# Performance work log

Measured on AMD Instinct MI355X. Metric: run time of the kernel, lower is better.

The kernel has to match this reference:

```python
import jax, jax.numpy as jnp
import numpy as np

N = 50000      # nodes
E = 800000     # edges (avg degree 16)
F_IN = 512
HID = 128
OUT = 40
DROPOUT = 0.5


def setup_inputs() -> dict:
    key = jax.random.key(0)
    ks = jax.random.split(key, 9)
    x = jax.random.normal(ks[0], (N, F_IN), dtype=jnp.float32)
    edge_src = jax.random.randint(ks[1], (E,), 0, N, dtype=jnp.int32)
    edge_dst = jax.random.randint(ks[2], (E,), 0, N, dtype=jnp.int32)
    edge_weight = jax.random.uniform(ks[3], (E,), dtype=jnp.float32)
    # GraphConvolution params (Glorot-ish init like the torch reference)
    s1 = 1.0 / np.sqrt(HID)
    W1 = jax.random.uniform(ks[4], (F_IN, HID), minval=-s1, maxval=s1, dtype=jnp.float32)
    b1 = jax.random.uniform(ks[5], (HID,), minval=-s1, maxval=s1, dtype=jnp.float32)
    s2 = 1.0 / np.sqrt(OUT)
    W2 = jax.random.uniform(ks[6], (HID, OUT), minval=-s2, maxval=s2, dtype=jnp.float32)
    b2 = jax.random.uniform(ks[7], (OUT,), minval=-s2, maxval=s2, dtype=jnp.float32)
    # Pre-sampled dropout mask (training-mode dropout, deterministic reference):
    keep = jax.random.bernoulli(ks[8], 1.0 - DROPOUT, (N, HID))
    drop_mask = keep.astype(jnp.float32) / (1.0 - DROPOUT)
    return {"x": x, "W1": W1, "b1": b1, "W2": W2, "b2": b2,
            "edge_weight": edge_weight, "drop_mask": drop_mask,
            "edge_src": edge_src, "edge_dst": edge_dst}


def spmm(edge_src, edge_dst, edge_weight, h):
    # out[i] = sum_{e: dst_e = i} w_e * h[src_e]   (sparse adj @ h)
    msgs = edge_weight[:, None] * h[edge_src]      # [E, d]
    return jax.ops.segment_sum(msgs, edge_dst, num_segments=N)


def reference(x, W1, b1, W2, b2, edge_weight, drop_mask, edge_src, edge_dst):
    # layer 1: adj @ (x @ W1) + b1, relu, dropout
    h = spmm(edge_src, edge_dst, edge_weight, x @ W1) + b1
    h = jax.nn.relu(h) * drop_mask
    # layer 2: adj @ (h @ W2) + b2
    out = spmm(edge_src, edge_dst, edge_weight, h @ W2) + b2
    return out
```

## Files before the change

### kernel.cpp

```cpp
#include <hip/hip_runtime.h>

#define NN 50000
#define NE 800000
#define FIN 512
#define HID 128
#define NOUT 40
#define H2P 64
#define CAP 64
#define NXS 16
#define GB1 782
#define EPB 2048
#define SB  391
#define MB  782

typedef __bf16 v8bf __attribute__((ext_vector_type(8)));
typedef float  v4f  __attribute__((ext_vector_type(4)));
typedef float  v2f  __attribute__((ext_vector_type(2)));
typedef unsigned short us8 __attribute__((ext_vector_type(8)));
typedef unsigned short us4 __attribute__((ext_vector_type(4)));
typedef unsigned int   u32x4 __attribute__((ext_vector_type(4)));
typedef unsigned int   u32x2 __attribute__((ext_vector_type(2)));

static __device__ __forceinline__ unsigned short f2bf(float f) {
  union { float f; unsigned int u; } v; v.f = f;
  unsigned int r = v.u + 0x7FFFu + ((v.u >> 16) & 1u);
  return (unsigned short)(r >> 16);
}
static __device__ __forceinline__ float bf2f(unsigned short s) {
  union { unsigned int u; float f; } v; v.u = ((unsigned int)s) << 16;
  return v.f;
}
static __device__ __forceinline__ float u2f(unsigned int u) {
  union { unsigned int u; float f; } v; v.u = u;
  return v.f;
}
static __device__ __forceinline__ v2f bfp2f(unsigned int u) {
  v2f r; r.x = u2f(u << 16); r.y = u2f(u & 0xFFFF0000u); return r;
}

__global__ void k_w1t(const float* __restrict__ W1, unsigned short* __restrict__ W1t,
                      int* __restrict__ nxt) {
  int id = blockIdx.x * 256 + threadIdx.x;
  int k = id >> 7;
  int n = id & 127;
  W1t[n * FIN + k] = f2bf(W1[k * HID + n]);
  if (id < NN) nxt[(size_t)id * NXS] = 0;
}

#define BM1 64
#define BK1 64
#define BKP1 72
__global__ __launch_bounds__(256) void k_fused(
    const float* __restrict__ x, const unsigned short* __restrict__ W1t,
    unsigned short* __restrict__ hb0,
    const int* __restrict__ src, const int* __restrict__ dst,
    const float* __restrict__ w, int* __restrict__ nxt,
    unsigned int* __restrict__ bkt,
    const float* __restrict__ mask, unsigned int* __restrict__ mpk) {
  __shared__ unsigned short As[BM1 * BKP1];
  __shared__ unsigned short Bs[HID * BKP1];
  const int t = threadIdx.x;

  if (blockIdx.x >= GB1 + SB) {
    int id = (blockIdx.x - (GB1 + SB)) * 256 + t;
    if (id < NN * 4) {
      int row = id >> 2, seg = id & 3;
      const float4* mp = (const float4*)(mask + (size_t)row * HID + seg * 32);
      unsigned int bits = 0;
      #pragma unroll
      for (int q = 0; q < 8; ++q) {
        float4 v = mp[q];
        bits |= (v.x != 0.f ? 1u : 0u) << (q * 4);
        bits |= (v.y != 0.f ? 1u : 0u) << (q * 4 + 1);
        bits |= (v.z != 0.f ? 1u : 0u) << (q * 4 + 2);
        bits |= (v.w != 0.f ? 1u : 0u) << (q * 4 + 3);
      }
      mpk[(size_t)row * 4 + seg] = bits;
    }
    return;
  }

  if (blockIdx.x >= GB1) {
    const int base = (blockIdx.x - GB1) * EPB + t;
    int   ii[8]; unsigned int pk[8]; int ok[8];
    #pragma unroll
    for (int k = 0; k < 8; ++k) {
      int e = base + k * 256;
      ok[k] = (e < NE);
      int ec = ok[k] ? e : (NE - 1);
      ii[k] = dst[ec];
      pk[k] = (unsigned int)src[ec] | ((unsigned int)f2bf(w[ec]) << 16);
    }
    int p[8];
    #pragma unroll
    for (int k = 0; k < 8; ++k)
      p[k] = ok[k] ? atomicAdd(&nxt[(size_t)ii[k] * NXS], 1) : CAP;
    #pragma unroll
    for (int k = 0; k < 8; ++k)
      if (p[k] < CAP) bkt[(size_t)ii[k] * CAP + p[k]] = pk[k];
    return;
  }

  const int r0 = blockIdx.x * BM1;
  const int wave = t >> 6, lane = t & 63;
  const int quad = lane >> 4, mr = lane & 15;
  const int mrow0 = (wave & 1) * 32;
  const int ncol0 = (wave >> 1) * 64;

  const int ar = t >> 2, aq = t & 3;
  int grow = r0 + ar; if (grow > NN - 1) grow = NN - 1;
  const float4* xrow = (const float4*)(x + (size_t)grow * FIN);
  const int bn = t >> 1, bh = t & 1;

  const v4f vzero = {0.f, 0.f, 0.f, 0.f};
  v4f acc[2][4];
  #pragma unroll
  for (int mi = 0; mi < 2; ++mi)
    #pragma unroll
    for (int j = 0; j < 4; ++j) acc[mi][j] = vzero;

  for (int k0 = 0; k0 < FIN; k0 += BK1) {
    float4 va[4];
    #pragma unroll
    for (int i = 0; i < 4; ++i) va[i] = xrow[(k0 >> 2) + aq + i * 4];
    us8 vb[4];
    const us8* bp = (const us8*)(W1t + bn * FIN + k0 + bh * 32);
    #pragma unroll
    for (int i = 0; i < 4; ++i) vb[i] = bp[i];

    __syncthreads();
    #pragma unroll
    for (int i = 0; i < 4; ++i) {
      us4 s; s.x = f2bf(va[i].x); s.y = f2bf(va[i].y);
             s.z = f2bf(va[i].z); s.w = f2bf(va[i].w);
      *(us4*)&As[ar * BKP1 + aq * 4 + i * 16] = s;
    }
    #pragma unroll
    for (int i = 0; i < 4; ++i)
      *(us8*)&Bs[bn * BKP1 + bh * 32 + i * 8] = vb[i];
    __syncthreads();

    #pragma unroll
    for (int ks = 0; ks < BK1; ks += 32) {
      v8bf a0 = *(const v8bf*)&As[(mrow0 + mr) * BKP1 + ks + quad * 8];
      v8bf a1 = *(const v8bf*)&As[(mrow0 + 16 + mr) * BKP1 + ks + quad * 8];
      #pragma unroll
      for (int j = 0; j < 4; ++j) {
        v8bf b = *(const v8bf*)&Bs[(ncol0 + j * 16 + mr) * BKP1 + ks + quad * 8];
        acc[0][j] = __builtin_amdgcn_mfma_f32_16x16x32_bf16(a0, b, acc[0][j], 0, 0, 0);
        acc[1][j] = __builtin_amdgcn_mfma_f32_16x16x32_bf16(a1, b, acc[1][j], 0, 0, 0);
      }
    }
  }

  #pragma unroll
  for (int mi = 0; mi < 2; ++mi)
    #pragma unroll
    for (int j = 0; j < 4; ++j)
      #pragma unroll
      for (int rr = 0; rr < 4; ++rr) {
        int row = r0 + mrow0 + mi * 16 + quad * 4 + rr;
        int col = ncol0 + j * 16 + mr;
        if (row < NN) hb0[(size_t)row * HID + col] = f2bf(acc[mi][j][rr]);
      }
}

__global__ __launch_bounds__(256) void k_spmm1(const unsigned short* __restrict__ hb0,
                                               const int* __restrict__ nxt,
                                               const unsigned int* __restrict__ bkt,
                                               const float* __restrict__ b1,
                                               const unsigned int* __restrict__ mpk,
                                               unsigned short* __restrict__ hb1) {
  const int t = threadIdx.x, lane = t & 63, wv = t >> 6;
  const int g = lane >> 4, ql = lane & 15;
  const int i = blockIdx.x * 4 + wv;
  const int c0 = ql * 8;
  int nE = nxt[(size_t)i * NXS]; if (nE > CAP) nE = CAP;
  const int m = (nE + 3 - g) >> 2;
  const unsigned int* ep = bkt + (size_t)i * CAP + g;

  const v2f z2 = {0.f, 0.f};
  v2f a0p[4] = {z2, z2, z2, z2};
  v2f a1p[4] = {z2, z2, z2, z2};
  int j = 0;
  for (; j + 3 < m; j += 4) {
    unsigned int p0 = ep[4*j], p1 = ep[4*j+4], p2 = ep[4*j+8], p3 = ep[4*j+12];
    int s0 = p0 & 0xFFFF, s1 = p1 & 0xFFFF, s2 = p2 & 0xFFFF, s3 = p3 & 0xFFFF;
    v2f w0 = {0.f, 0.f}, w1 = w0, w2 = w0, w3 = w0;
    w0.x = w0.y = bf2f((unsigned short)(p0 >> 16));
    w1.x = w1.y = bf2f((unsigned short)(p1 >> 16));
    w2.x = w2.y = bf2f((unsigned short)(p2 >> 16));
    w3.x = w3.y = bf2f((unsigned short)(p3 >> 16));
    u32x4 h0 = *(const u32x4*)&hb0[(size_t)s0 * HID + c0];
    u32x4 h1 = *(const u32x4*)&hb0[(size_t)s1 * HID + c0];
    u32x4 h2 = *(const u32x4*)&hb0[(size_t)s2 * HID + c0];
    u32x4 h3 = *(const u32x4*)&hb0[(size_t)s3 * HID + c0];
    #pragma unroll
    for (int d = 0; d < 4; ++d) {
      a0p[d] += w0 * bfp2f(h0[d]);
      a1p[d] += w1 * bfp2f(h1[d]);
      a0p[d] += w2 * bfp2f(h2[d]);
      a1p[d] += w3 * bfp2f(h3[d]);
    }
  }
  for (; j < m; ++j) {
    unsigned int p = ep[4*j];
    int s = p & 0xFFFF;
    v2f w; w.x = w.y = bf2f((unsigned short)(p >> 16));
    u32x4 h = *(const u32x4*)&hb0[(size_t)s * HID + c0];
    #pragma unroll
    for (int d = 0; d < 4; ++d) a0p[d] += w * bfp2f(h[d]);
  }
  float v[8];
  #pragma unroll
  for (int d = 0; d < 4; ++d) {
    v2f s = a0p[d] + a1p[d];
    v[2*d] = s.x; v[2*d+1] = s.y;
  }
  #pragma unroll
  for (int k = 0; k < 8; ++k) {
    v[k] += __shfl_xor(v[k], 16);
    v[k] += __shfl_xor(v[k], 32);
  }
  if (g == 0) {
    unsigned int word = mpk[(size_t)i * 4 + (ql >> 2)];
    unsigned int byte = (word >> ((ql & 3) * 8)) & 0xFFu;
    const float4 bbA = *(const float4*)&b1[c0];
    const float4 bbB = *(const float4*)&b1[c0 + 4];
    float bb[8] = {bbA.x, bbA.y, bbA.z, bbA.w, bbB.x, bbB.y, bbB.z, bbB.w};
    us8 o;
    #pragma unroll
    for (int k = 0; k < 8; ++k) {
      float r = ((byte >> k) & 1u) ? fmaxf(v[k] + bb[k], 0.f) * 2.0f : 0.f;
      o[k] = f2bf(r);
    }
    *(us8*)&hb1[(size_t)i * HID + c0] = o;
  }
}

#define BKP2 136
__global__ __launch_bounds__(256) void k_gemm2(const unsigned short* __restrict__ hb1,
                                               const float* __restrict__ W2,
                                               unsigned short* __restrict__ h2b) {
  __shared__ unsigned short As[64 * BKP2];
  __shared__ unsigned short Bs[48 * BKP2];
  const int t = threadIdx.x;
  const int r0 = blockIdx.x * 64;
  const int wave = t >> 6, lane = t & 63;
  const int quad = lane >> 4, mr = lane & 15;
  const int mrow0 = wave * 16;

  const int ar = t >> 2, aq = t & 3;
  int grow = r0 + ar; if (grow > NN - 1) grow = NN - 1;
  const us8* hrow = (const us8*)(hb1 + (size_t)grow * HID);
  #pragma unroll
  for (int i = 0; i < 4; ++i) {
    us8 v = hrow[aq + i * 4];
    *(us8*)&As[ar * BKP2 + aq * 8 + i * 32] = v;
  }
  if (t < 192) {
    int n = t >> 2, q = t & 3;
    #pragma unroll
    for (int kk = 0; kk < 32; ++kk) {
      int k = q * 32 + kk;
      float val = (n < NOUT) ? W2[k * NOUT + n] : 0.f;
      Bs[n * BKP2 + k] = f2bf(val);
    }
  }
  __syncthreads();

  const v4f vzero = {0.f, 0.f, 0.f, 0.f};
  v4f acc[3] = {vzero, vzero, vzero};
  #pragma unroll
  for (int ks = 0; ks < HID; ks += 32) {
    v8bf a = *(const v8bf*)&As[(mrow0 + mr) * BKP2 + ks + quad * 8];
    #pragma unroll
    for (int j = 0; j < 3; ++j) {
      v8bf b = *(const v8bf*)&Bs[(j * 16 + mr) * BKP2 + ks + quad * 8];
      acc[j] = __builtin_amdgcn_mfma_f32_16x16x32_bf16(a, b, acc[j], 0, 0, 0);
    }
  }
  #pragma unroll
  for (int j = 0; j < 3; ++j)
    #pragma unroll
    for (int rr = 0; rr < 4; ++rr) {
      int row = r0 + mrow0 + quad * 4 + rr;
      int col = j * 16 + mr;
      if (row < NN && col < NOUT) h2b[(size_t)row * H2P + col] = f2bf(acc[j][rr]);
    }
}

__global__ __launch_bounds__(256) void k_spmm2(const unsigned short* __restrict__ h2b,
                                               const int* __restrict__ nxt,
                                               const unsigned int* __restrict__ bkt,
                                               const float* __restrict__ b2,
                                               float* __restrict__ out) {
  const int t = threadIdx.x, lane = t & 63;
  const int g = lane >> 4, ql = lane & 15;
  const int i = blockIdx.x * 4 + (t >> 6);
  if (i >= NN) return;
  const int act = (ql < 10);
  const int c0 = act ? ql * 4 : 0;
  int nE = nxt[(size_t)i * NXS]; if (nE > CAP) nE = CAP;
  const int m = (nE + 3 - g) >> 2;
  const unsigned int* ep = bkt + (size_t)i * CAP + g;

  const v2f z2 = {0.f, 0.f};
  v2f a0p[2] = {z2, z2};
  v2f a1p[2] = {z2, z2};
  int j = 0;
  for (; j + 3 < m; j += 4) {
    unsigned int p0 = ep[4*j], p1 = ep[4*j+4], p2 = ep[4*j+8], p3 = ep[4*j+12];
    int s0 = p0 & 0xFFFF, s1 = p1 & 0xFFFF, s2 = p2 & 0xFFFF, s3 = p3 & 0xFFFF;
    v2f w0, w1, w2, w3;
    w0.x = w0.y = bf2f((unsigned short)(p0 >> 16));
    w1.x = w1.y = bf2f((unsigned short)(p1 >> 16));
    w2.x = w2.y = bf2f((unsigned short)(p2 >> 16));
    w3.x = w3.y = bf2f((unsigned short)(p3 >> 16));
    u32x2 h0 = *(const u32x2*)&h2b[(size_t)s0 * H2P + c0];
    u32x2 h1 = *(const u32x2*)&h2b[(size_t)s1 * H2P + c0];
    u32x2 h2 = *(const u32x2*)&h2b[(size_t)s2 * H2P + c0];
    u32x2 h3 = *(const u32x2*)&h2b[(size_t)s3 * H2P + c0];
    #pragma unroll
    for (int d = 0; d < 2; ++d) {
      a0p[d] += w0 * bfp2f(h0[d]);
      a1p[d] += w1 * bfp2f(h1[d]);
      a0p[d] += w2 * bfp2f(h2[d]);
      a1p[d] += w3 * bfp2f(h3[d]);
    }
  }
  for (; j < m; ++j) {
    unsigned int p = ep[4*j];
    int s = p & 0xFFFF;
    v2f w; w.x = w.y = bf2f((unsigned short)(p >> 16));
    u32x2 h = *(const u32x2*)&h2b[(size_t)s * H2P + c0];
    #pragma unroll
    for (int d = 0; d < 2; ++d) a0p[d] += w * bfp2f(h[d]);
  }
  float v[4];
  #pragma unroll
  for (int d = 0; d < 2; ++d) {
    v2f s = a0p[d] + a1p[d];
    v[2*d] = s.x; v[2*d+1] = s.y;
  }
  #pragma unroll
  for (int k = 0; k < 4; ++k) {
    v[k] += __shfl_xor(v[k], 16);
    v[k] += __shfl_xor(v[k], 32);
  }
  if (g == 0 && act) {
    const float4 bb = *(const float4*)&b2[c0];
    float4 o;
    o.x = v[0] + bb.x;
    o.y = v[1] + bb.y;
    o.z = v[2] + bb.z;
    o.w = v[3] + bb.w;
    *(float4*)&out[(size_t)i * NOUT + c0] = o;
  }
}

extern "C" void kernel_launch(void* const* d_in, const int* in_sizes, int n_in,
                              void* d_out, int out_size, void* d_ws, size_t ws_size,
                              hipStream_t stream) {
  const float* x   = (const float*)d_in[0];
  const float* W1  = (const float*)d_in[1];
  const float* b1  = (const float*)d_in[2];
  const float* W2  = (const float*)d_in[3];
  const float* b2  = (const float*)d_in[4];
  const float* ew  = (const float*)d_in[5];
  const float* msk = (const float*)d_in[6];
  const int* esrc  = (const int*)d_in[7];
  const int* edst  = (const int*)d_in[8];
  float* out = (float*)d_out;

  char* ws = (char*)d_ws;
  unsigned short* hb0 = (unsigned short*)ws; ws += (size_t)NN * HID * 2;
  unsigned short* hb1 = (unsigned short*)ws; ws += (size_t)NN * HID * 2;
  unsigned short* h2b = (unsigned short*)ws; ws += (size_t)NN * H2P * 2;
  unsigned short* W1t = (unsigned short*)ws; ws += (size_t)HID * FIN * 2;
  unsigned int* bkt   = (unsigned int*)ws;   ws += (size_t)NN * CAP * 4;
  unsigned int* mpk   = (unsigned int*)ws;   ws += (size_t)NN * 4 * 4;
  int* nxt            = (int*)ws;            ws += (size_t)NN * NXS * 4;

  k_w1t  <<<(FIN * HID) / 256, 256, 0, stream>>>(W1, W1t, nxt);
  k_fused<<<GB1 + SB + MB, 256, 0, stream>>>(x, W1t, hb0,
                                             esrc, edst, ew, nxt, bkt,
                                             msk, mpk);
  k_spmm1<<<NN / 4, 256, 0, stream>>>(hb0, nxt, bkt, b1, mpk, hb1);
  k_gemm2<<<(NN + 63) / 64, 256, 0, stream>>>(hb1, W2, h2b);
  k_spmm2<<<(NN + 3) / 4, 256, 0, stream>>>(h2b, nxt, bkt, b2, out);
}
```

Measured before the change: 295.4 us.

## Load GEMM operands directly from global into MFMA registers, dropping LDS staging

The x@W1 GEMM in the fused kernel no longer stages tiles of x and W1t through shared memory with barriers. Each lane now loads its own MFMA fragments straight from global memory, converting x to bf16 in registers, over a fully unrolled K loop. This removes LDS traffic and __syncthreads, but the two waves sharing a row slice (or column slice) each fetch it from global, relying on cache for reuse. The per-lane accesses are also less coalesced (16-byte chunks spread across rows) and register pressure rises from the full unroll.

```diff
diff --git a/kernel.cpp b/kernel.cpp
--- a/kernel.cpp
+++ b/kernel.cpp
@@ -48,8 +48,6 @@
 }
 
 #define BM1 64
-#define BK1 64
-#define BKP1 72
 __global__ __launch_bounds__(256) void k_fused(
     const float* __restrict__ x, const unsigned short* __restrict__ W1t,
     unsigned short* __restrict__ hb0,
@@ -57,8 +55,6 @@
     const float* __restrict__ w, int* __restrict__ nxt,
     unsigned int* __restrict__ bkt,
     const float* __restrict__ mask, unsigned int* __restrict__ mpk) {
-  __shared__ unsigned short As[BM1 * BKP1];
-  __shared__ unsigned short Bs[HID * BKP1];
   const int t = threadIdx.x;
 
   if (blockIdx.x >= GB1 + SB) {
@@ -107,10 +103,14 @@
   const int mrow0 = (wave & 1) * 32;
   const int ncol0 = (wave >> 1) * 64;
 
-  const int ar = t >> 2, aq = t & 3;
-  int grow = r0 + ar; if (grow > NN - 1) grow = NN - 1;
-  const float4* xrow = (const float4*)(x + (size_t)grow * FIN);
-  const int bn = t >> 1, bh = t & 1;
+  int rA0 = r0 + mrow0 + mr;      if (rA0 > NN - 1) rA0 = NN - 1;
+  int rA1 = r0 + mrow0 + 16 + mr; if (rA1 > NN - 1) rA1 = NN - 1;
+  const float* xr0 = x + (size_t)rA0 * FIN;
+  const float* xr1 = x + (size_t)rA1 * FIN;
+  const unsigned short* wb0 = W1t + (size_t)(ncol0 + 0 * 16 + mr) * FIN;
+  const unsigned short* wb1 = W1t + (size_t)(ncol0 + 1 * 16 + mr) * FIN;
+  const unsigned short* wb2 = W1t + (size_t)(ncol0 + 2 * 16 + mr) * FIN;
+  const unsigned short* wb3 = W1t + (size_t)(ncol0 + 3 * 16 + mr) * FIN;
 
   const v4f vzero = {0.f, 0.f, 0.f, 0.f};
   v4f acc[2][4];
@@ -119,38 +119,34 @@
     #pragma unroll
     for (int j = 0; j < 4; ++j) acc[mi][j] = vzero;
 
-  for (int k0 = 0; k0 < FIN; k0 += BK1) {
-    float4 va[4];
-    #pragma unroll
-    for (int i = 0; i < 4; ++i) va[i] = xrow[(k0 >> 2) + aq + i * 4];
-    us8 vb[4];
-    const us8* bp = (const us8*)(W1t + bn * FIN + k0 + bh * 32);
-    #pragma unroll
-    for (int i = 0; i < 4; ++i) vb[i] = bp[i];
-
-    __syncthreads();
-    #pragma unroll
-    for (int i = 0; i < 4; ++i) {
-      us4 s; s.x = f2bf(va[i].x); s.y = f2bf(va[i].y);
-             s.z = f2bf(va[i].z); s.w = f2bf(va[i].w);
-      *(us4*)&As[ar * BKP1 + aq * 4 + i * 16] = s;
-    }
-    #pragma unroll
-    for (int i = 0; i < 4; ++i)
-      *(us8*)&Bs[bn * BKP1 + bh * 32 + i * 8] = vb[i];
-    __syncthreads();
-
-    #pragma unroll
-    for (int ks = 0; ks < BK1; ks += 32) {
-      v8bf a0 = *(const v8bf*)&As[(mrow0 + mr) * BKP1 + ks + quad * 8];
-      v8bf a1 = *(const v8bf*)&As[(mrow0 + 16 + mr) * BKP1 + ks + quad * 8];
-      #pragma unroll
-      for (int j = 0; j < 4; ++j) {
-        v8bf b = *(const v8bf*)&Bs[(ncol0 + j * 16 + mr) * BKP1 + ks + quad * 8];
-        acc[0][j] = __builtin_amdgcn_mfma_f32_16x16x32_bf16(a0, b, acc[0][j], 0, 0, 0);
-        acc[1][j] = __builtin_amdgcn_mfma_f32_16x16x32_bf16(a1, b, acc[1][j], 0, 0, 0);
-      }
-    }
+  #pragma unroll
+  for (int kk = 0; kk < 16; ++kk) {
+    const int k = kk * 32 + quad * 8;
+    float4 a0lo = *(const float4*)(xr0 + k);
+    float4 a0hi = *(const float4*)(xr0 + k + 4);
+    float4 a1lo = *(const float4*)(xr1 + k);
+    float4 a1hi = *(const float4*)(xr1 + k + 4);
+    v8bf b0 = *(const v8bf*)(wb0 + k);
+    v8bf b1 = *(const v8bf*)(wb1 + k);
+    v8bf b2 = *(const v8bf*)(wb2 + k);
+    v8bf b3 = *(const v8bf*)(wb3 + k);
+    v8bf A0, A1;
+    A0[0] = (__bf16)a0lo.x; A0[1] = (__bf16)a0lo.y;
+    A0[2] = (__bf16)a0lo.z; A0[3] = (__bf16)a0lo.w;
+    A0[4] = (__bf16)a0hi.x; A0[5] = (__bf16)a0hi.y;
+    A0[6] = (__bf16)a0hi.z; A0[7] = (__bf16)a0hi.w;
+    A1[0] = (__bf16)a1lo.x; A1[1] = (__bf16)a1lo.y;
+    A1[2] = (__bf16)a1lo.z; A1[3] = (__bf16)a1lo.w;
+    A1[4] = (__bf16)a1hi.x; A1[5] = (__bf16)a1hi.y;
+    A1[6] = (__bf16)a1hi.z; A1[7] = (__bf16)a1hi.w;
+    acc[0][0] = __builtin_amdgcn_mfma_f32_16x16x32_bf16(A0, b0, acc[0][0], 0, 0, 0);
+    acc[1][0] = __builtin_amdgcn_mfma_f32_16x16x32_bf16(A1, b0, acc[1][0], 0, 0, 0);
+    acc[0][1] = __builtin_amdgcn_mfma_f32_16x16x32_bf16(A0, b1, acc[0][1], 0, 0, 0);
+    acc[1][1] = __builtin_amdgcn_mfma_f32_16x16x32_bf16(A1, b1, acc[1][1], 0, 0, 0);
+    acc[0][2] = __builtin_amdgcn_mfma_f32_16x16x32_bf16(A0, b2, acc[0][2], 0, 0, 0);
+    acc[1][2] = __builtin_amdgcn_mfma_f32_16x16x32_bf16(A1, b2, acc[1][2], 0, 0, 0);
+    acc[0][3] = __builtin_amdgcn_mfma_f32_16x16x32_bf16(A0, b3, acc[0][3], 0, 0, 0);
+    acc[1][3] = __builtin_amdgcn_mfma_f32_16x16x32_bf16(A1, b3, acc[1][3], 0, 0, 0);
   }
 
   #pragma unroll
```

New measurement: 323.3 us. 1.09x slower.
